# Kernel optimization log

Measured on AMD Instinct MI355X. Metric: run time of the kernel, lower is better.

Reference implementation:

```python
import jax, jax.numpy as jnp
import numpy as np

N = 100000      # nodes
E = 1600000     # edges (avg degree 16)
IN = 128        # in_feats
H = 4           # num_heads
F = 32          # out_feats per head
NEG_SLOPE = 0.2


def setup_inputs() -> dict:
    key = jax.random.key(0)
    k0, k1, k2, k3, k4, k5 = jax.random.split(key, 6)
    feat = jax.random.normal(k0, (N, IN), dtype=jnp.float32)
    # Glorot-ish scaled params
    W = jax.random.normal(k1, (IN, H * F), dtype=jnp.float32) * (1.0 / np.sqrt(IN))
    attn_l = jax.random.normal(k2, (H, F), dtype=jnp.float32) * 0.1
    attn_r = jax.random.normal(k3, (H, F), dtype=jnp.float32) * 0.1
    bias = jnp.zeros((H * F,), dtype=jnp.float32)
    src = jax.random.randint(k4, (E,), 0, N, dtype=jnp.int32)
    dst = jax.random.randint(k5, (E,), 0, N, dtype=jnp.int32)
    return {"feat": feat, "W": W, "attn_l": attn_l, "attn_r": attn_r,
            "bias": bias, "src": src, "dst": dst}


def reference(feat, W, attn_l, attn_r, bias, src, dst):
    # GeMM: projected features, [N, H, F]
    feat_src = (feat @ W).reshape(N, H, F)
    # per-node attention halves, [N, H]
    el = (feat_src * attn_l).sum(-1)
    er = (feat_src * attn_r).sum(-1)
    # per-edge score e_ij = LeakyReLU(el[src] + er[dst]), [E, H]
    e = el[src] + er[dst]
    e = jnp.where(e > 0, e, NEG_SLOPE * e)
    # edge softmax over destination-node segments (numerically stable)
    m = jax.ops.segment_max(e, dst, num_segments=N)          # [N, H]
    ex = jnp.exp(e - m[dst])                                  # [E, H]
    denom = jax.ops.segment_sum(ex, dst, num_segments=N)     # [N, H]
    alpha = ex / jnp.maximum(denom[dst], 1e-9)                # [E, H]
    # weighted SpMM aggregation: sum_j alpha_ij * Wh_j, [N, H, F]
    msg = feat_src[src] * alpha[:, :, None]                   # [E, H, F]
    rst = jax.ops.segment_sum(msg, dst, num_segments=N)      # [N, H, F]
    rst = rst + bias.reshape(1, H, F)
    return rst
```

## Files before the change

kernel.cpp:

```cpp
#include <hip/hip_runtime.h>

#define IN_F 128
#define HF   128
#define NH   4
#define NF   32

#define NPB       256
#define NPB_SHIFT 8
#define BIN_CHUNK 4096

typedef __attribute__((ext_vector_type(8))) short short8v;
typedef __attribute__((ext_vector_type(4))) float f32x4;

__device__ __forceinline__ unsigned short f32_to_bf16_rtn(float f) {
    unsigned int u = __float_as_uint(f);
    u += 0x7fffu + ((u >> 16) & 1u);
    return (unsigned short)(u >> 16);
}
__device__ __forceinline__ float bf16_lo(unsigned int u) { return __uint_as_float(u << 16); }
__device__ __forceinline__ float bf16_hi(unsigned int u) { return __uint_as_float(u & 0xffff0000u); }

__global__ void __launch_bounds__(256)
gat_wfrag(const float* __restrict__ W, short8v* __restrict__ wfrag) {
    const int entry = blockIdx.x * 256 + threadIdx.x;
    const int lane = entry & 63;
    const int kb   = (entry >> 6) & 3;
    const int nt   = entry >> 8;
    const int k0   = kb * 32 + (lane >> 4) * 8;
    const int col  = nt * 16 + (lane & 15);
    short8v s;
    #pragma unroll
    for (int j = 0; j < 8; ++j)
        s[j] = (short)f32_to_bf16_rtn(W[(k0 + j) * HF + col]);
    wfrag[entry] = s;
}

__global__ void __launch_bounds__(256)
gat_gemm_mfma(const float* __restrict__ feat, const short8v* __restrict__ wfrag,
              const float* __restrict__ attn_l, const float* __restrict__ attn_r,
              unsigned short* __restrict__ feat_src_bf,
              float* __restrict__ el, float* __restrict__ er, int N) {
    __shared__ unsigned short a_lds[8192];
    __shared__ unsigned short w_lds[16384];
    const int t    = threadIdx.x;
    const int lane = t & 63;
    const int wave = t >> 6;
    const int row0b = blockIdx.x * 64;

    {
        const uint4* wsrc = (const uint4*)wfrag;
        uint4* wdst = (uint4*)w_lds;
        #pragma unroll
        for (int i = 0; i < 8; ++i)
            wdst[i * 256 + t] = wsrc[i * 256 + t];
    }
    #pragma unroll
    for (int i = 0; i < 8; ++i) {
        int idx = i * 256 + t;
        int row = idx >> 5;
        int c4  = idx & 31;
        int srow = min(row0b + row, N - 1);
        float4 f = *(const float4*)(feat + (size_t)srow * IN_F + c4 * 4);
        unsigned int lo = ((unsigned int)f32_to_bf16_rtn(f.y) << 16) | f32_to_bf16_rtn(f.x);
        unsigned int hi = ((unsigned int)f32_to_bf16_rtn(f.w) << 16) | f32_to_bf16_rtn(f.z);
        int kb = c4 >> 3, g = (c4 >> 1) & 3, half = c4 & 1;
        int wv = row >> 4, m = row & 15;
        unsigned int* p = (unsigned int*)a_lds;
        int u = (wv * 4096 + kb * 1024 + g * 256 + m * 16 + half * 8) >> 2;
        p[u]     = lo;
        p[u + 1] = hi;
    }
    __syncthreads();

    const int m = lane & 15;
    const int g = lane >> 4;
    short8v aw[4];
    #pragma unroll
    for (int kb = 0; kb < 4; ++kb)
        aw[kb] = *(const short8v*)&a_lds[wave * 2048 + kb * 512 + g * 128 + m * 8];

    f32x4 acc[8];
    #pragma unroll
    for (int nt = 0; nt < 8; ++nt) acc[nt] = (f32x4){0.f, 0.f, 0.f, 0.f};

    #pragma unroll
    for (int nt = 0; nt < 8; ++nt) {
        #pragma unroll
        for (int kb = 0; kb < 4; ++kb) {
            short8v bw = *(const short8v*)&w_lds[((nt * 4 + kb) * 64 + lane) * 8];
            acc[nt] = __builtin_amdgcn_mfma_f32_16x16x32_bf16(aw[kb], bw, acc[nt], 0, 0, 0);
        }
    }

    float al[8], ar[8];
    #pragma unroll
    for (int nt = 0; nt < 8; ++nt) {
        al[nt] = attn_l[nt * 16 + m];
        ar[nt] = attn_r[nt * 16 + m];
    }

    #pragma unroll
    for (int r = 0; r < 4; ++r) {
        const int row = row0b + wave * 16 + 4 * g + r;
        const bool valid = (row < N);
        if (valid) {
            #pragma unroll
            for (int nt = 0; nt < 8; ++nt)
                feat_src_bf[(size_t)row * HF + nt * 16 + m] = f32_to_bf16_rtn(acc[nt][r]);
        }
        float pl[NH], pr[NH];
        #pragma unroll
        for (int h = 0; h < NH; ++h) {
            pl[h] = acc[2 * h][r] * al[2 * h] + acc[2 * h + 1][r] * al[2 * h + 1];
            pr[h] = acc[2 * h][r] * ar[2 * h] + acc[2 * h + 1][r] * ar[2 * h + 1];
        }
        #pragma unroll
        for (int mask = 1; mask <= 8; mask <<= 1) {
            #pragma unroll
            for (int h = 0; h < NH; ++h) {
                pl[h] += __shfl_xor(pl[h], mask);
                pr[h] += __shfl_xor(pr[h], mask);
            }
        }
        if (valid && m == 0) {
            *(float4*)(el + (size_t)row * NH) = make_float4(pl[0], pl[1], pl[2], pl[3]);
            *(float4*)(er + (size_t)row * NH) = make_float4(pr[0], pr[1], pr[2], pr[3]);
        }
    }
}

__global__ void __launch_bounds__(256)
gat_bucket_hist(const int* __restrict__ dst, int* __restrict__ bcount,
                int E, int nbuck, int chunk) {
    __shared__ int h[512];
    const int t = threadIdx.x;
    for (int i = t; i < 512; i += 256) h[i] = 0;
    __syncthreads();
    const int e0 = blockIdx.x * chunk;
    const int e1 = min(e0 + chunk, E);
    for (int e = e0 + t; e < e1; e += 256)
        atomicAdd(&h[dst[e] >> NPB_SHIFT], 1);
    __syncthreads();
    for (int b = t; b < nbuck; b += 256)
        if (h[b]) atomicAdd(&bcount[b], h[b]);
}

__global__ void __launch_bounds__(512)
gat_bucket_scan(const int* __restrict__ bcount, int* __restrict__ bbase,
                int* __restrict__ gcursor, int* __restrict__ offsets,
                int N, int E, int nbuck) {
    __shared__ int buf[512];
    const int t = threadIdx.x;
    int v = (t < nbuck) ? bcount[t] : 0;
    buf[t] = v;
    __syncthreads();
    for (int off = 1; off < 512; off <<= 1) {
        int x = (t >= off) ? buf[t - off] : 0;
        __syncthreads();
        buf[t] += x;
        __syncthreads();
    }
    if (t < nbuck) {
        int base = buf[t] - v;
        bbase[t]   = base;
        gcursor[t] = base;
    }
    if (t == 0) {
        bbase[nbuck] = E;
        offsets[N]   = E;
    }
}

__global__ void __launch_bounds__(256)
gat_bin(const int* __restrict__ src, const int* __restrict__ dst,
        int* __restrict__ gcursor, unsigned int* __restrict__ gpairs, int E) {
    __shared__ unsigned int stage[BIN_CHUNK];
    __shared__ unsigned short buckof[BIN_CHUNK];
    __shared__ int hist[512];
    __shared__ int sc[512];
    __shared__ int basew[512];
    __shared__ int cur[512];
    const int t = threadIdx.x;
    for (int i = t; i < 512; i += 256) hist[i] = 0;
    __syncthreads();
    const int e0  = blockIdx.x * BIN_CHUNK;
    const int cnt = min(BIN_CHUNK, E - e0);
    for (int i = t; i < cnt; i += 256)
        atomicAdd(&hist[dst[e0 + i] >> NPB_SHIFT], 1);
    __syncthreads();
    sc[t]       = hist[t];
    sc[t + 256] = hist[t + 256];
    __syncthreads();
    for (int off = 1; off < 512; off <<= 1) {
        int x0 = (t >= off) ? sc[t - off] : 0;
        int x1 = sc[t + 256 - off];
        __syncthreads();
        sc[t]       += x0;
        sc[t + 256] += x1;
        __syncthreads();
    }
    for (int b = t; b < 512; b += 256) {
        int c  = hist[b];
        int ex = sc[b] - c;
        cur[b] = ex;
        basew[b] = c ? atomicAdd(&gcursor[b], c) : 0;
    }
    __syncthreads();
    for (int i = t; i < cnt; i += 256) {
        unsigned s = (unsigned)src[e0 + i];
        unsigned d = (unsigned)dst[e0 + i];
        int b = (int)(d >> NPB_SHIFT);
        int p = atomicAdd(&cur[b], 1);
        stage[p]  = (s << 8) | (d & (NPB - 1));
        buckof[p] = (unsigned short)b;
    }
    __syncthreads();
    for (int j = t; j < cnt; j += 256) {
        int b  = (int)buckof[j];
        int ex = sc[b] - hist[b];
        gpairs[basew[b] + (j - ex)] = stage[j];
    }
}

__global__ void __launch_bounds__(256)
gat_fine(const unsigned int* __restrict__ gpairs, const int* __restrict__ bbase,
         int* __restrict__ offsets, int* __restrict__ slot, int N) {
    __shared__ int h[NPB];
    __shared__ int buf[NPB];
    __shared__ int cur[NPB];
    const int b     = blockIdx.x;
    const int node0 = b << NPB_SHIFT;
    const int t     = threadIdx.x;
    const int beg = bbase[b];
    const int end = bbase[b + 1];
    h[t] = 0;
    __syncthreads();
    for (int i = beg + t; i < end; i += 256)
        atomicAdd(&h[gpairs[i] & (NPB - 1)], 1);
    __syncthreads();
    int v = h[t];
    buf[t] = v;
    __syncthreads();
    for (int off = 1; off < 256; off <<= 1) {
        int x = (t >= off) ? buf[t - off] : 0;
        __syncthreads();
        buf[t] += x;
        __syncthreads();
    }
    int ex = buf[t] - v;
    if (node0 + t < N) offsets[node0 + t] = beg + ex;
    cur[t] = ex;
    __syncthreads();
    for (int i = beg + t; i < end; i += 256) {
        unsigned pr = gpairs[i];
        int p = atomicAdd(&cur[pr & (NPB - 1)], 1);
        slot[beg + p] = (int)(pr >> 8);
    }
}

__global__ void __launch_bounds__(256)
gat_aggregate(const unsigned short* __restrict__ feat_src_bf,
              const float* __restrict__ el, const float* __restrict__ er,
              const int* __restrict__ offsets, const int* __restrict__ slot,
              const float* __restrict__ bias, float* __restrict__ out, int N) {
    __shared__ int   ss[4][64];
    __shared__ float exs[4][256];
    const int lane = threadIdx.x & 63;
    const int wave = threadIdx.x >> 6;
    const int node = blockIdx.x * 4 + wave;
    if (node >= N) return;
    const int start = offsets[node];
    const int end   = offsets[node + 1];
    const int k  = lane & 15;
    const int g  = lane >> 4;
    const int hm = k >> 2;

    const float4 er4 = *(const float4*)(er + (size_t)node * NH);
    float d0 = 0.f, d1 = 0.f, d2 = 0.f, d3 = 0.f;
    float ax0 = 0.f, ax1 = 0.f, ax2 = 0.f, ax3 = 0.f;
    float ax4 = 0.f, ax5 = 0.f, ax6 = 0.f, ax7 = 0.f;
    const unsigned short* fsp = feat_src_bf + 8 * k;
    int*   ssw = ss[wave];
    float* exw = exs[wave];

    for (int c = start; c < end; c += 64) {
        int idx = c + lane;
        bool vld = idx < end;
        int s_l = vld ? slot[idx] : 0;
        float4 ev = make_float4(0.f, 0.f, 0.f, 0.f);
        if (vld) ev = *(const float4*)(el + (size_t)s_l * NH);
        float x0 = ev.x + er4.x; x0 = fmaxf(x0, 0.2f * x0);
        float x1 = ev.y + er4.y; x1 = fmaxf(x1, 0.2f * x1);
        float x2 = ev.z + er4.z; x2 = fmaxf(x2, 0.2f * x2);
        float x3 = ev.w + er4.w; x3 = fmaxf(x3, 0.2f * x3);
        float e0 = vld ? __expf(x0) : 0.f;
        float e1 = vld ? __expf(x1) : 0.f;
        float e2 = vld ? __expf(x2) : 0.f;
        float e3 = vld ? __expf(x3) : 0.f;
        d0 += e0; d1 += e1; d2 += e2; d3 += e3;
        ssw[lane] = s_l;
        *(float4*)&exw[lane * 4] = make_float4(e0, e1, e2, e3);
        asm volatile("" ::: "memory");
        const int n = min(64, end - c);
        int j = g;
        for (; j + 4 < n; j += 8) {
            int jB = j + 4;
            int sA = ssw[j];
            int sB = ssw[jB];
            float wA = exw[j * 4 + hm];
            float wB = exw[jB * 4 + hm];
            uint4 uA = *(const uint4*)(fsp + (size_t)sA * HF);
            uint4 uB = *(const uint4*)(fsp + (size_t)sB * HF);
            ax0 += wA * bf16_lo(uA.x) + wB * bf16_lo(uB.x);
            ax1 += wA * bf16_hi(uA.x) + wB * bf16_hi(uB.x);
            ax2 += wA * bf16_lo(uA.y) + wB * bf16_lo(uB.y);
            ax3 += wA * bf16_hi(uA.y) + wB * bf16_hi(uB.y);
            ax4 += wA * bf16_lo(uA.z) + wB * bf16_lo(uB.z);
            ax5 += wA * bf16_hi(uA.z) + wB * bf16_hi(uB.z);
            ax6 += wA * bf16_lo(uA.w) + wB * bf16_lo(uB.w);
            ax7 += wA * bf16_hi(uA.w) + wB * bf16_hi(uB.w);
        }
        if (j < n) {
            int sA = ssw[j];
            float wA = exw[j * 4 + hm];
            uint4 uA = *(const uint4*)(fsp + (size_t)sA * HF);
            ax0 += wA * bf16_lo(uA.x);
            ax1 += wA * bf16_hi(uA.x);
            ax2 += wA * bf16_lo(uA.y);
            ax3 += wA * bf16_hi(uA.y);
            ax4 += wA * bf16_lo(uA.z);
            ax5 += wA * bf16_hi(uA.z);
            ax6 += wA * bf16_lo(uA.w);
            ax7 += wA * bf16_hi(uA.w);
        }
        asm volatile("" ::: "memory");
    }

    #pragma unroll
    for (int msk = 16; msk <= 32; msk <<= 1) {
        ax0 += __shfl_xor(ax0, msk); ax1 += __shfl_xor(ax1, msk);
        ax2 += __shfl_xor(ax2, msk); ax3 += __shfl_xor(ax3, msk);
        ax4 += __shfl_xor(ax4, msk); ax5 += __shfl_xor(ax5, msk);
        ax6 += __shfl_xor(ax6, msk); ax7 += __shfl_xor(ax7, msk);
    }

    #pragma unroll
    for (int msk = 1; msk <= 32; msk <<= 1) {
        d0 += __shfl_xor(d0, msk);
        d1 += __shfl_xor(d1, msk);
        d2 += __shfl_xor(d2, msk);
        d3 += __shfl_xor(d3, msk);
    }
    float dh = (hm == 0) ? d0 : (hm == 1) ? d1 : (hm == 2) ? d2 : d3;
    const float inv = 1.0f / fmaxf(dh, 1e-9f);

    if (g == 0) {
        float4 b0 = *(const float4*)(bias + 8 * k);
        float4 b1 = *(const float4*)(bias + 8 * k + 4);
        float4 o0, o1;
        o0.x = ax0 * inv + b0.x; o0.y = ax1 * inv + b0.y;
        o0.z = ax2 * inv + b0.z; o0.w = ax3 * inv + b0.w;
        o1.x = ax4 * inv + b1.x; o1.y = ax5 * inv + b1.y;
        o1.z = ax6 * inv + b1.z; o1.w = ax7 * inv + b1.w;
        *(float4*)(out + (size_t)node * HF + 8 * k)     = o0;
        *(float4*)(out + (size_t)node * HF + 8 * k + 4) = o1;
    }
}

extern "C" void kernel_launch(void* const* d_in, const int* in_sizes, int n_in,
                              void* d_out, int out_size, void* d_ws, size_t ws_size,
                              hipStream_t stream) {
    const float* feat   = (const float*)d_in[0];
    const float* W      = (const float*)d_in[1];
    const float* attn_l = (const float*)d_in[2];
    const float* attn_r = (const float*)d_in[3];
    const float* bias   = (const float*)d_in[4];
    const int*   src    = (const int*)d_in[5];
    const int*   dst    = (const int*)d_in[6];
    float* out = (float*)d_out;

    const int N = in_sizes[0] / IN_F;
    const int E = in_sizes[5];
    const int nbuck = (N + NPB - 1) / NPB;

    char* ws = (char*)d_ws;
    size_t off = 0;
    auto alloc = [&](size_t bytes) -> void* {
        off = (off + 255) & ~(size_t)255;
        void* p = ws + off;
        off += bytes;
        return p;
    };
    unsigned short* feat_src_bf = (unsigned short*)alloc((size_t)N * HF * sizeof(unsigned short));
    float* el      = (float*)alloc((size_t)N * NH * sizeof(float));
    float* er      = (float*)alloc((size_t)N * NH * sizeof(float));
    int*   bcount  = (int*)  alloc((size_t)(nbuck + 1) * sizeof(int));
    int*   bbase   = (int*)  alloc((size_t)(nbuck + 1) * sizeof(int));
    int*   gcursor = (int*)  alloc((size_t)nbuck * sizeof(int));
    int*   offsets = (int*)  alloc((size_t)(N + 1) * sizeof(int));
    unsigned int* gpairs = (unsigned int*)alloc((size_t)E * sizeof(unsigned int));
    int*   slot    = (int*)  alloc((size_t)E * sizeof(int));
    short8v* wfrag = (short8v*)alloc((size_t)2048 * sizeof(short8v));

    hipMemsetAsync(bcount, 0, (size_t)(nbuck + 1) * sizeof(int), stream);

    gat_wfrag<<<8, 256, 0, stream>>>(W, wfrag);
    gat_gemm_mfma<<<(N + 63) / 64, 256, 0, stream>>>(
        feat, wfrag, attn_l, attn_r, feat_src_bf, el, er, N);

    const int nwg1   = 256;
    const int chunk1 = (E + nwg1 - 1) / nwg1;
    gat_bucket_hist<<<nwg1, 256, 0, stream>>>(dst, bcount, E, nbuck, chunk1);
    gat_bucket_scan<<<1, 512, 0, stream>>>(bcount, bbase, gcursor, offsets, N, E, nbuck);
    gat_bin<<<(E + BIN_CHUNK - 1) / BIN_CHUNK, 256, 0, stream>>>(src, dst, gcursor, gpairs, E);
    gat_fine<<<nbuck, 256, 0, stream>>>(gpairs, bbase, offsets, slot, N);

    gat_aggregate<<<(N + 3) / 4, 256, 0, stream>>>(feat_src_bf, el, er, offsets, slot, bias, out, N);
}
```

Baseline: 156.3 us.

## Fuse bucket histogram into GEMM launch and unroll aggregation gather by four

The destination-bucket histogram kernel is merged into the projection GEMM launch: the first 256 blocks compute the histogram and the rest run the GEMM, so the two independent jobs share one launch and can overlap on the GPU. Shared memory becomes a single 48 KB buffer sliced per role, which could affect occupancy for the histogram blocks. Separately, the aggregation inner loop gains a 4-way unrolled gather path so more feature-row loads are in flight per iteration, at the cost of higher register pressure.

Result: faster. 151.6 us (-3.0%).

```diff
diff --git a/kernel.cpp b/kernel.cpp
--- a/kernel.cpp
+++ b/kernel.cpp
@@ -8,6 +8,7 @@
 #define NPB       256
 #define NPB_SHIFT 8
 #define BIN_CHUNK 4096
+#define HIST_BLOCKS 256
 
 typedef __attribute__((ext_vector_type(8))) short short8v;
 typedef __attribute__((ext_vector_type(4))) float f32x4;
@@ -36,16 +37,34 @@
 }
 
 __global__ void __launch_bounds__(256)
-gat_gemm_mfma(const float* __restrict__ feat, const short8v* __restrict__ wfrag,
+gat_gemm_hist(const float* __restrict__ feat, const short8v* __restrict__ wfrag,
               const float* __restrict__ attn_l, const float* __restrict__ attn_r,
               unsigned short* __restrict__ feat_src_bf,
-              float* __restrict__ el, float* __restrict__ er, int N) {
-    __shared__ unsigned short a_lds[8192];
-    __shared__ unsigned short w_lds[16384];
-    const int t    = threadIdx.x;
+              float* __restrict__ el, float* __restrict__ er, int N,
+              const int* __restrict__ dst, int* __restrict__ bcount,
+              int E, int nbuck, int chunk) {
+    __shared__ __align__(16) char smem[49152];
+    const int t = threadIdx.x;
+
+    if ((int)blockIdx.x < HIST_BLOCKS) {
+        int* h = (int*)smem;
+        for (int i = t; i < 512; i += 256) h[i] = 0;
+        __syncthreads();
+        const int e0 = blockIdx.x * chunk;
+        const int e1 = min(e0 + chunk, E);
+        for (int e = e0 + t; e < e1; e += 256)
+            atomicAdd(&h[dst[e] >> NPB_SHIFT], 1);
+        __syncthreads();
+        for (int b = t; b < nbuck; b += 256)
+            if (h[b]) atomicAdd(&bcount[b], h[b]);
+        return;
+    }
+
+    unsigned short* a_lds = (unsigned short*)smem;
+    unsigned short* w_lds = (unsigned short*)(smem + 16384);
     const int lane = t & 63;
     const int wave = t >> 6;
-    const int row0b = blockIdx.x * 64;
+    const int row0b = (blockIdx.x - HIST_BLOCKS) * 64;
 
     {
         const uint4* wsrc = (const uint4*)wfrag;
@@ -127,22 +146,6 @@
             *(float4*)(er + (size_t)row * NH) = make_float4(pr[0], pr[1], pr[2], pr[3]);
         }
     }
-}
-
-__global__ void __launch_bounds__(256)
-gat_bucket_hist(const int* __restrict__ dst, int* __restrict__ bcount,
-                int E, int nbuck, int chunk) {
-    __shared__ int h[512];
-    const int t = threadIdx.x;
-    for (int i = t; i < 512; i += 256) h[i] = 0;
-    __syncthreads();
-    const int e0 = blockIdx.x * chunk;
-    const int e1 = min(e0 + chunk, E);
-    for (int e = e0 + t; e < e1; e += 256)
-        atomicAdd(&h[dst[e] >> NPB_SHIFT], 1);
-    __syncthreads();
-    for (int b = t; b < nbuck; b += 256)
-        if (h[b]) atomicAdd(&bcount[b], h[b]);
 }
 
 __global__ void __launch_bounds__(512)
@@ -303,6 +306,29 @@
         asm volatile("" ::: "memory");
         const int n = min(64, end - c);
         int j = g;
+        for (; j + 12 < n; j += 16) {
+            int j1 = j + 4, j2 = j + 8, j3 = j + 12;
+            int sA = ssw[j];
+            int sB = ssw[j1];
+            int sC = ssw[j2];
+            int sD = ssw[j3];
+            float wA = exw[j  * 4 + hm];
+            float wB = exw[j1 * 4 + hm];
+            float wC = exw[j2 * 4 + hm];
+            float wD = exw[j3 * 4 + hm];
+            uint4 uA = *(const uint4*)(fsp + (size_t)sA * HF);
+            uint4 uB = *(const uint4*)(fsp + (size_t)sB * HF);
+            uint4 uC = *(const uint4*)(fsp + (size_t)sC * HF);
+            uint4 uD = *(const uint4*)(fsp + (size_t)sD * HF);
+            ax0 += wA * bf16_lo(uA.x) + wB * bf16_lo(uB.x) + wC * bf16_lo(uC.x) + wD * bf16_lo(uD.x);
+            ax1 += wA * bf16_hi(uA.x) + wB * bf16_hi(uB.x) + wC * bf16_hi(uC.x) + wD * bf16_hi(uD.x);
+            ax2 += wA * bf16_lo(uA.y) + wB * bf16_lo(uB.y) + wC * bf16_lo(uC.y) + wD * bf16_lo(uD.y);
+            ax3 += wA * bf16_hi(uA.y) + wB * bf16_hi(uB.y) + wC * bf16_hi(uC.y) + wD * bf16_hi(uD.y);
+            ax4 += wA * bf16_lo(uA.z) + wB * bf16_lo(uB.z) + wC * bf16_lo(uC.z) + wD * bf16_lo(uD.z);
+            ax5 += wA * bf16_hi(uA.z) + wB * bf16_hi(uB.z) + wC * bf16_hi(uC.z) + wD * bf16_hi(uD.z);
+            ax6 += wA * bf16_lo(uA.w) + wB * bf16_lo(uB.w) + wC * bf16_lo(uC.w) + wD * bf16_lo(uD.w);
+            ax7 += wA * bf16_hi(uA.w) + wB * bf16_hi(uB.w) + wC * bf16_hi(uC.w) + wD * bf16_hi(uD.w);
+        }
         for (; j + 4 < n; j += 8) {
             int jB = j + 4;
             int sA = ssw[j];
@@ -405,12 +431,13 @@
     hipMemsetAsync(bcount, 0, (size_t)(nbuck + 1) * sizeof(int), stream);
 
     gat_wfrag<<<8, 256, 0, stream>>>(W, wfrag);
-    gat_gemm_mfma<<<(N + 63) / 64, 256, 0, stream>>>(
-        feat, wfrag, attn_l, attn_r, feat_src_bf, el, er, N);
-
-    const int nwg1   = 256;
-    const int chunk1 = (E + nwg1 - 1) / nwg1;
-    gat_bucket_hist<<<nwg1, 256, 0, stream>>>(dst, bcount, E, nbuck, chunk1);
+
+    const int gemmBlocks = (N + 63) / 64;
+    const int chunk1 = (E + HIST_BLOCKS - 1) / HIST_BLOCKS;
+    gat_gemm_hist<<<HIST_BLOCKS + gemmBlocks, 256, 0, stream>>>(
+        feat, wfrag, attn_l, attn_r, feat_src_bf, el, er, N,
+        dst, bcount, E, nbuck, chunk1);
+
     gat_bucket_scan<<<1, 512, 0, stream>>>(bcount, bbase, gcursor, offsets, N, E, nbuck);
     gat_bin<<<(E + BIN_CHUNK - 1) / BIN_CHUNK, 256, 0, stream>>>(src, dst, gcursor, gpairs, E);
     gat_fine<<<nbuck, 256, 0, stream>>>(gpairs, bbase, offsets, slot, N);
```
